# Optimization experiments

Hardware: AMD Instinct MI355X
Metric: run time of the kernel (lower is better)

## Reference

```python
import jax, jax.numpy as jnp
import numpy as np

B, N, F = 4, 3000, 128

def setup_inputs() -> dict:
    key = jax.random.key(0)
    k1, k2, k3, k4 = jax.random.split(key, 4)
    x = jax.random.normal(k1, (B, N, F), dtype=jnp.float32)
    adj = jax.random.uniform(k2, (B, N, N), dtype=jnp.float32)
    h0 = jax.random.normal(k3, (B, N, F), dtype=jnp.float32)
    stdv = 1.0 / np.sqrt(F)
    theta = jax.random.uniform(k4, (F, F), dtype=jnp.float32, minval=-stdv, maxval=stdv)
    return {
        "x": x, "adj": adj, "h0": h0, "theta": theta,
        "lamda": jnp.float32(0.5), "alpha": jnp.float32(0.1), "l": 4,
    }

def _normalize_adj(adj):
    # add self loops, then D^{-1/2} A D^{-1/2} via elementwise row/col scaling
    # (same math as diag-embed + inverse + two bmms in the original)
    n = adj.shape[1]
    adj = adj + jnp.eye(n, dtype=adj.dtype)
    deg = jnp.sum(adj, axis=2)                      # [B, N]
    d_inv_sqrt = jax.lax.rsqrt(deg)                 # [B, N]
    return d_inv_sqrt[:, :, None] * adj * d_inv_sqrt[:, None, :]

def reference(x, adj, h0, theta, lamda, alpha, l):
    adj_n = _normalize_adj(adj)
    beta = jnp.log(lamda / l + 1.0)
    hi = jnp.einsum('bnm,bmf->bnf', adj_n, x)       # aggregation
    support = (1.0 - alpha) * hi + alpha * h0       # variant=False path
    r = support
    out = beta * jnp.einsum('bnf,fg->bng', support, theta) + (1.0 - beta) * r
    return out
```

## Files before the change

### kernel.cpp

```cpp
#include <hip/hip_runtime.h>
#include <hip/hip_bf16.h>
#include <math.h>

#define BB 4
#define NN 3000
#define FF 128
#define NKC 94
#define NIT 188

typedef __bf16 bf16x8 __attribute__((ext_vector_type(8)));
typedef __bf16 bf16x4 __attribute__((ext_vector_type(4)));
typedef float  f32x4  __attribute__((ext_vector_type(4)));

__global__ __launch_bounds__(256) void k_deg(const float* __restrict__ adj,
                                             float* __restrict__ dis) {
    int wid  = (blockIdx.x * 256 + threadIdx.x) >> 6;
    int lane = threadIdx.x & 63;
    if (wid >= BB * NN) return;
    const float4* row = (const float4*)(adj + (size_t)wid * NN);
    float s = 0.f;
    for (int c = lane; c < NN / 4; c += 64) {
        float4 v = row[c];
        s += (v.x + v.y) + (v.z + v.w);
    }
    for (int off = 32; off > 0; off >>= 1) s += __shfl_down(s, off, 64);
    if (lane == 0) dis[wid] = 1.0f / sqrtf(s + 1.0f);
}

__global__ __launch_bounds__(256) void k_xpk(const float* __restrict__ x,
                                             const float* __restrict__ dis,
                                             __bf16* __restrict__ xpk) {
    int b  = blockIdx.y, kc = blockIdx.x;
    int t  = threadIdx.x, w = t >> 6, l = t & 63;
    int m  = l & 15, q = l >> 4;
    #pragma unroll
    for (int h = 0; h < 2; ++h) {
        int nt = w + h * 4;
        int f  = nt * 16 + m;
        bf16x8 v;
        #pragma unroll
        for (int j = 0; j < 8; ++j) {
            int k = kc * 32 + q * 8 + j;
            float val = 0.f;
            if (k < NN) val = dis[b * NN + k] * x[((size_t)b * NN + k) * FF + f];
            v[j] = (__bf16)val;
        }
        *(bf16x8*)(xpk + ((size_t)(b * 8 + nt) * NKC + kc) * 512 + l * 8) = v;
    }
}

__global__ __launch_bounds__(256) void k_thpk(const float* __restrict__ theta,
                                              __bf16* __restrict__ thpk) {
    int kc = blockIdx.x;
    int t  = threadIdx.x, w = t >> 6, l = t & 63;
    int m  = l & 15, q = l >> 4;
    #pragma unroll
    for (int h = 0; h < 2; ++h) {
        int nt = w + h * 4;
        bf16x8 v;
        #pragma unroll
        for (int j = 0; j < 8; ++j) {
            int k = kc * 32 + q * 8 + j;
            v[j] = (__bf16)theta[k * FF + nt * 16 + m];
        }
        *(bf16x8*)(thpk + ((size_t)(nt * 4 + kc)) * 512 + l * 8) = v;
    }
}

__global__ __launch_bounds__(256) void k_agg(const float* __restrict__ adj,
                                             const __bf16* __restrict__ xpk,
                                             const __bf16* __restrict__ thpk,
                                             const float* __restrict__ x,
                                             const float* __restrict__ h0,
                                             const float* __restrict__ dis,
                                             float* __restrict__ out,
                                             const float* __restrict__ alpha_p,
                                             const float* __restrict__ lamda_p,
                                             const int* __restrict__ l_p) {
    __shared__ __bf16 tile[16][264];
    const int b  = blockIdx.y;
    const int i0 = blockIdx.x * 16;
    const int t  = threadIdx.x, w = t >> 6, l = t & 63;
    const int m  = l & 15, quad = l >> 4;
    const int n0 = w * 32;
    const __bf16* B0 = xpk + ((size_t)(b * 8 + 2 * w) * NKC) * 512 + l * 8;
    const __bf16* B1 = B0 + (size_t)NKC * 512;
    f32x4 acc0 = {0.f, 0.f, 0.f, 0.f};
    f32x4 acc1 = {0.f, 0.f, 0.f, 0.f};
    for (int c = 0; c < 12; ++c) {
        int k0 = c * 256;
        #pragma unroll
        for (int i = 0; i < 4; ++i) {
            int row = i * 4 + w;
            int col = k0 + l * 4;
            float4 v = {0.f, 0.f, 0.f, 0.f};
            if (i0 + row < NN && col < NN)
                v = *(const float4*)(adj + ((size_t)b * NN + i0 + row) * NN + col);
            __bf16* tp = &tile[row][l * 4];
            tp[0] = (__bf16)v.x; tp[1] = (__bf16)v.y;
            tp[2] = (__bf16)v.z; tp[3] = (__bf16)v.w;
        }
        __syncthreads();
        int nk = (c == 11) ? 6 : 8;
        #pragma unroll 2
        for (int kcl = 0; kcl < nk; ++kcl) {
            int kc = c * 8 + kcl;
            bf16x8 a  = *(const bf16x8*)&tile[m][kcl * 32 + quad * 8];
            bf16x8 b0 = *(const bf16x8*)(B0 + (size_t)kc * 512);
            bf16x8 b1 = *(const bf16x8*)(B1 + (size_t)kc * 512);
            acc0 = __builtin_amdgcn_mfma_f32_16x16x32_bf16(a, b0, acc0, 0, 0, 0);
            acc1 = __builtin_amdgcn_mfma_f32_16x16x32_bf16(a, b1, acc1, 0, 0, 0);
        }
        __syncthreads();
    }
    const float alpha = *alpha_p;
    const float beta  = logf(*lamda_p / (float)(*l_p) + 1.0f);
    float s0v[4], s1v[4];
    #pragma unroll
    for (int r = 0; r < 4; ++r) {
        int row  = quad * 4 + r;
        int irow = i0 + row;
        float s0 = 0.f, s1 = 0.f;
        if (irow < NN) {
            float  di   = dis[b * NN + irow];
            size_t base = ((size_t)b * NN + irow) * FF;
            int c0 = n0 + m, c1 = n0 + 16 + m;
            s0 = (1.f - alpha) * (di * acc0[r] + di * di * x[base + c0]) + alpha * h0[base + c0];
            s1 = (1.f - alpha) * (di * acc1[r] + di * di * x[base + c1]) + alpha * h0[base + c1];
        }
        s0v[r] = s0; s1v[r] = s1;
        tile[row][n0 + m]      = (__bf16)s0;
        tile[row][n0 + 16 + m] = (__bf16)s1;
    }
    __syncthreads();
    f32x4 o0 = {0.f, 0.f, 0.f, 0.f};
    f32x4 o1 = {0.f, 0.f, 0.f, 0.f};
    const __bf16* T0 = thpk + (size_t)(2 * w * 4) * 512 + l * 8;
    const __bf16* T1 = T0 + 4 * 512;
    #pragma unroll
    for (int kc = 0; kc < 4; ++kc) {
        bf16x8 a   = *(const bf16x8*)&tile[m][kc * 32 + quad * 8];
        bf16x8 tb0 = *(const bf16x8*)(T0 + (size_t)kc * 512);
        bf16x8 tb1 = *(const bf16x8*)(T1 + (size_t)kc * 512);
        o0 = __builtin_amdgcn_mfma_f32_16x16x32_bf16(a, tb0, o0, 0, 0, 0);
        o1 = __builtin_amdgcn_mfma_f32_16x16x32_bf16(a, tb1, o1, 0, 0, 0);
    }
    const float omb = 1.f - beta;
    #pragma unroll
    for (int r = 0; r < 4; ++r) {
        int irow = i0 + quad * 4 + r;
        if (irow < NN) {
            size_t base = ((size_t)b * NN + irow) * FF;
            out[base + n0 + m]      = beta * o0[r] + omb * s0v[r];
            out[base + n0 + 16 + m] = beta * o1[r] + omb * s1v[r];
        }
    }
}

extern "C" void kernel_launch(void* const* d_in, const int* in_sizes, int n_in,
                              void* d_out, int out_size, void* d_ws, size_t ws_size,
                              hipStream_t stream) {
    const float* x      = (const float*)d_in[0];
    const float* adj    = (const float*)d_in[1];
    const float* h0     = (const float*)d_in[2];
    const float* theta  = (const float*)d_in[3];
    const float* lamda  = (const float*)d_in[4];
    const float* alpha  = (const float*)d_in[5];
    const int*   l      = (const int*)d_in[6];
    float* out = (float*)d_out;

    char*   ws   = (char*)d_ws;
    float*  dis  = (float*)ws;
    __bf16* xpk  = (__bf16*)(ws + 65536);
    __bf16* thpk = (__bf16*)(ws + 3200000);

    k_deg<<<dim3((BB * NN) / 4), 256, 0, stream>>>(adj, dis);
    k_xpk<<<dim3(NKC, BB), 256, 0, stream>>>(x, dis, xpk);
    k_thpk<<<dim3(4), 256, 0, stream>>>(theta, thpk);
    k_agg<<<dim3(NIT, BB), 256, 0, stream>>>(adj, xpk, thpk, x, h0, dis, out,
                                             alpha, lamda, l);
}
```

Measured before the change: 287.0 us.

## Fuse degree pass with bf16 MFMA-fragment packing of adjacency

The row-sum degree kernel is replaced by one that streams each 16-row adjacency tile once. It computes the row degrees and writes the tile as bf16 in the exact per-lane MFMA A-fragment layout. The aggregation kernel then loads A fragments straight from global memory, with no LDS staging, fp32-to-bf16 conversion or per-chunk barriers in its main loop. This moves the conversion work out of the GEMM loop and halves the bytes the GEMM reads for adjacency. In exchange it adds a 72 MB bf16 write and read-back through the workspace, which must be large enough to hold it.

```diff
diff --git a/kernel.cpp b/kernel.cpp
--- a/kernel.cpp
+++ b/kernel.cpp
@@ -9,22 +9,53 @@
 #define NIT 188
 
 typedef __bf16 bf16x8 __attribute__((ext_vector_type(8)));
-typedef __bf16 bf16x4 __attribute__((ext_vector_type(4)));
 typedef float  f32x4  __attribute__((ext_vector_type(4)));
 
-__global__ __launch_bounds__(256) void k_deg(const float* __restrict__ adj,
-                                             float* __restrict__ dis) {
-    int wid  = (blockIdx.x * 256 + threadIdx.x) >> 6;
-    int lane = threadIdx.x & 63;
-    if (wid >= BB * NN) return;
-    const float4* row = (const float4*)(adj + (size_t)wid * NN);
-    float s = 0.f;
-    for (int c = lane; c < NN / 4; c += 64) {
-        float4 v = row[c];
-        s += (v.x + v.y) + (v.z + v.w);
+__global__ __launch_bounds__(256) void k_degpack(const float* __restrict__ adj,
+                                                 __bf16* __restrict__ apk,
+                                                 float* __restrict__ dis) {
+    __shared__ float tile[16][260];
+    const int b  = blockIdx.y;
+    const int it = blockIdx.x;
+    const int i0 = it * 16;
+    const int t  = threadIdx.x, w = t >> 6, l = t & 63;
+    const int m  = l & 15, quad = l >> 4;
+    float dreg[4] = {0.f, 0.f, 0.f, 0.f};
+    __bf16* dst = apk + ((size_t)(b * NIT + it) * NKC) * 512 + l * 8;
+    for (int c = 0; c < 12; ++c) {
+        int k0 = c * 256;
+        #pragma unroll
+        for (int i = 0; i < 4; ++i) {
+            int row = i * 4 + w;
+            int col = k0 + l * 4;
+            float4 v = {0.f, 0.f, 0.f, 0.f};
+            if (i0 + row < NN && col < NN)
+                v = *(const float4*)(adj + ((size_t)b * NN + i0 + row) * NN + col);
+            dreg[i] += (v.x + v.y) + (v.z + v.w);
+            *(float4*)&tile[row][l * 4] = v;
+        }
+        __syncthreads();
+        int nk = (c == 11) ? 6 : 8;
+        #pragma unroll
+        for (int h = 0; h < 2; ++h) {
+            int kcl = w + h * 4;
+            if (kcl < nk) {
+                bf16x8 a;
+                #pragma unroll
+                for (int j = 0; j < 8; ++j)
+                    a[j] = (__bf16)tile[m][kcl * 32 + quad * 8 + j];
+                *(bf16x8*)(dst + (size_t)(c * 8 + kcl) * 512) = a;
+            }
+        }
+        __syncthreads();
     }
-    for (int off = 32; off > 0; off >>= 1) s += __shfl_down(s, off, 64);
-    if (lane == 0) dis[wid] = 1.0f / sqrtf(s + 1.0f);
+    #pragma unroll
+    for (int i = 0; i < 4; ++i) {
+        float s = dreg[i];
+        for (int off = 32; off > 0; off >>= 1) s += __shfl_down(s, off, 64);
+        int irow = i0 + i * 4 + w;
+        if (l == 0 && irow < NN) dis[b * NN + irow] = 1.0f / sqrtf(s + 1.0f);
+    }
 }
 
 __global__ __launch_bounds__(256) void k_xpk(const float* __restrict__ x,
@@ -67,7 +98,7 @@
     }
 }
 
-__global__ __launch_bounds__(256) void k_agg(const float* __restrict__ adj,
+__global__ __launch_bounds__(256) void k_agg(const __bf16* __restrict__ apk,
                                              const __bf16* __restrict__ xpk,
                                              const __bf16* __restrict__ thpk,
                                              const float* __restrict__ x,
@@ -77,41 +108,25 @@
                                              const float* __restrict__ alpha_p,
                                              const float* __restrict__ lamda_p,
                                              const int* __restrict__ l_p) {
-    __shared__ __bf16 tile[16][264];
+    __shared__ __bf16 stile[16][136];
     const int b  = blockIdx.y;
-    const int i0 = blockIdx.x * 16;
+    const int it = blockIdx.x;
+    const int i0 = it * 16;
     const int t  = threadIdx.x, w = t >> 6, l = t & 63;
     const int m  = l & 15, quad = l >> 4;
     const int n0 = w * 32;
+    const __bf16* Ap = apk + ((size_t)(b * NIT + it) * NKC) * 512 + l * 8;
     const __bf16* B0 = xpk + ((size_t)(b * 8 + 2 * w) * NKC) * 512 + l * 8;
     const __bf16* B1 = B0 + (size_t)NKC * 512;
     f32x4 acc0 = {0.f, 0.f, 0.f, 0.f};
     f32x4 acc1 = {0.f, 0.f, 0.f, 0.f};
-    for (int c = 0; c < 12; ++c) {
-        int k0 = c * 256;
-        #pragma unroll
-        for (int i = 0; i < 4; ++i) {
-            int row = i * 4 + w;
-            int col = k0 + l * 4;
-            float4 v = {0.f, 0.f, 0.f, 0.f};
-            if (i0 + row < NN && col < NN)
-                v = *(const float4*)(adj + ((size_t)b * NN + i0 + row) * NN + col);
-            __bf16* tp = &tile[row][l * 4];
-            tp[0] = (__bf16)v.x; tp[1] = (__bf16)v.y;
-            tp[2] = (__bf16)v.z; tp[3] = (__bf16)v.w;
-        }
-        __syncthreads();
-        int nk = (c == 11) ? 6 : 8;
-        #pragma unroll 2
-        for (int kcl = 0; kcl < nk; ++kcl) {
-            int kc = c * 8 + kcl;
-            bf16x8 a  = *(const bf16x8*)&tile[m][kcl * 32 + quad * 8];
-            bf16x8 b0 = *(const bf16x8*)(B0 + (size_t)kc * 512);
-            bf16x8 b1 = *(const bf16x8*)(B1 + (size_t)kc * 512);
-            acc0 = __builtin_amdgcn_mfma_f32_16x16x32_bf16(a, b0, acc0, 0, 0, 0);
-            acc1 = __builtin_amdgcn_mfma_f32_16x16x32_bf16(a, b1, acc1, 0, 0, 0);
-        }
-        __syncthreads();
+    #pragma unroll 2
+    for (int kc = 0; kc < NKC; ++kc) {
+        bf16x8 a  = *(const bf16x8*)(Ap + (size_t)kc * 512);
+        bf16x8 b0 = *(const bf16x8*)(B0 + (size_t)kc * 512);
+        bf16x8 b1 = *(const bf16x8*)(B1 + (size_t)kc * 512);
+        acc0 = __builtin_amdgcn_mfma_f32_16x16x32_bf16(a, b0, acc0, 0, 0, 0);
+        acc1 = __builtin_amdgcn_mfma_f32_16x16x32_bf16(a, b1, acc1, 0, 0, 0);
     }
     const float alpha = *alpha_p;
     const float beta  = logf(*lamda_p / (float)(*l_p) + 1.0f);
@@ -129,8 +144,8 @@
             s1 = (1.f - alpha) * (di * acc1[r] + di * di * x[base + c1]) + alpha * h0[base + c1];
         }
         s0v[r] = s0; s1v[r] = s1;
-        tile[row][n0 + m]      = (__bf16)s0;
-        tile[row][n0 + 16 + m] = (__bf16)s1;
+        stile[row][n0 + m]      = (__bf16)s0;
+        stile[row][n0 + 16 + m] = (__bf16)s1;
     }
     __syncthreads();
     f32x4 o0 = {0.f, 0.f, 0.f, 0.f};
@@ -139,7 +154,7 @@
     const __bf16* T1 = T0 + 4 * 512;
     #pragma unroll
     for (int kc = 0; kc < 4; ++kc) {
-        bf16x8 a   = *(const bf16x8*)&tile[m][kc * 32 + quad * 8];
+        bf16x8 a   = *(const bf16x8*)&stile[m][kc * 32 + quad * 8];
         bf16x8 tb0 = *(const bf16x8*)(T0 + (size_t)kc * 512);
         bf16x8 tb1 = *(const bf16x8*)(T1 + (size_t)kc * 512);
         o0 = __builtin_amdgcn_mfma_f32_16x16x32_bf16(a, tb0, o0, 0, 0, 0);
@@ -173,10 +188,11 @@
     float*  dis  = (float*)ws;
     __bf16* xpk  = (__bf16*)(ws + 65536);
     __bf16* thpk = (__bf16*)(ws + 3200000);
+    __bf16* apk  = (__bf16*)(ws + 4 * 1024 * 1024);
 
-    k_deg<<<dim3((BB * NN) / 4), 256, 0, stream>>>(adj, dis);
+    k_degpack<<<dim3(NIT, BB), 256, 0, stream>>>(adj, apk, dis);
+    k_thpk<<<dim3(4), 256, 0, stream>>>(theta, thpk);
     k_xpk<<<dim3(NKC, BB), 256, 0, stream>>>(x, dis, xpk);
-    k_thpk<<<dim3(4), 256, 0, stream>>>(theta, thpk);
-    k_agg<<<dim3(NIT, BB), 256, 0, stream>>>(adj, xpk, thpk, x, h0, dis, out,
+    k_agg<<<dim3(NIT, BB), 256, 0, stream>>>(apk, xpk, thpk, x, h0, dis, out,
                                              alpha, lamda, l);
 }
```

Result: no change. 287.3 us (+0.1%).

## Double-buffer adjacency tiles with register prefetch in aggregation kernel

Applied to the files above, without the earlier changes.

The aggregation kernel now uses two shared-memory buffers of 512 columns each. The next adjacency chunk is loaded into registers while MFMAs run on the current buffer, which halves the number of barriers and overlaps global loads with compute. NKC is padded to 96 so the chunk loop divides evenly, and zero-filled packed x covers the padding. Shared memory and register use go up, which may lower occupancy.

```diff
diff --git a/kernel.cpp b/kernel.cpp
--- a/kernel.cpp
+++ b/kernel.cpp
@@ -5,11 +5,10 @@
 #define BB 4
 #define NN 3000
 #define FF 128
-#define NKC 94
+#define NKC 96
 #define NIT 188
 
 typedef __bf16 bf16x8 __attribute__((ext_vector_type(8)));
-typedef __bf16 bf16x4 __attribute__((ext_vector_type(4)));
 typedef float  f32x4  __attribute__((ext_vector_type(4)));
 
 __global__ __launch_bounds__(256) void k_deg(const float* __restrict__ adj,
@@ -77,9 +76,11 @@
                                              const float* __restrict__ alpha_p,
                                              const float* __restrict__ lamda_p,
                                              const int* __restrict__ l_p) {
-    __shared__ __bf16 tile[16][264];
+    __shared__ __bf16 tile[2][16][520];
+    __shared__ __bf16 stile[16][136];
     const int b  = blockIdx.y;
-    const int i0 = blockIdx.x * 16;
+    const int it = blockIdx.x;
+    const int i0 = it * 16;
     const int t  = threadIdx.x, w = t >> 6, l = t & 63;
     const int m  = l & 15, quad = l >> 4;
     const int n0 = w * 32;
@@ -87,32 +88,56 @@
     const __bf16* B1 = B0 + (size_t)NKC * 512;
     f32x4 acc0 = {0.f, 0.f, 0.f, 0.f};
     f32x4 acc1 = {0.f, 0.f, 0.f, 0.f};
-    for (int c = 0; c < 12; ++c) {
-        int k0 = c * 256;
+
+    float4 pu[4], pv[4];
+    auto load_chunk = [&](int c) {
+        int k0 = c * 512;
+        #pragma unroll
+        for (int i = 0; i < 4; ++i) {
+            int row  = i * 4 + w;
+            int irow = i0 + row;
+            int col  = k0 + l * 8;
+            float4 u = {0.f, 0.f, 0.f, 0.f}, v = {0.f, 0.f, 0.f, 0.f};
+            if (irow < NN && col < NN) {
+                const float* p = adj + ((size_t)b * NN + irow) * NN + col;
+                u = *(const float4*)p;
+                v = *(const float4*)(p + 4);
+            }
+            pu[i] = u; pv[i] = v;
+        }
+    };
+    auto store_chunk = [&](int cb) {
         #pragma unroll
         for (int i = 0; i < 4; ++i) {
             int row = i * 4 + w;
-            int col = k0 + l * 4;
-            float4 v = {0.f, 0.f, 0.f, 0.f};
-            if (i0 + row < NN && col < NN)
-                v = *(const float4*)(adj + ((size_t)b * NN + i0 + row) * NN + col);
-            __bf16* tp = &tile[row][l * 4];
-            tp[0] = (__bf16)v.x; tp[1] = (__bf16)v.y;
-            tp[2] = (__bf16)v.z; tp[3] = (__bf16)v.w;
-        }
-        __syncthreads();
-        int nk = (c == 11) ? 6 : 8;
-        #pragma unroll 2
-        for (int kcl = 0; kcl < nk; ++kcl) {
-            int kc = c * 8 + kcl;
-            bf16x8 a  = *(const bf16x8*)&tile[m][kcl * 32 + quad * 8];
+            bf16x8 s;
+            s[0] = (__bf16)pu[i].x; s[1] = (__bf16)pu[i].y;
+            s[2] = (__bf16)pu[i].z; s[3] = (__bf16)pu[i].w;
+            s[4] = (__bf16)pv[i].x; s[5] = (__bf16)pv[i].y;
+            s[6] = (__bf16)pv[i].z; s[7] = (__bf16)pv[i].w;
+            *(bf16x8*)&tile[cb][row][l * 8] = s;
+        }
+    };
+
+    load_chunk(0);
+    store_chunk(0);
+    __syncthreads();
+    for (int c = 0; c < 6; ++c) {
+        int cb = c & 1;
+        if (c < 5) load_chunk(c + 1);
+        #pragma unroll 4
+        for (int kcl = 0; kcl < 16; ++kcl) {
+            int kc = c * 16 + kcl;
+            bf16x8 a  = *(const bf16x8*)&tile[cb][m][kcl * 32 + quad * 8];
             bf16x8 b0 = *(const bf16x8*)(B0 + (size_t)kc * 512);
             bf16x8 b1 = *(const bf16x8*)(B1 + (size_t)kc * 512);
             acc0 = __builtin_amdgcn_mfma_f32_16x16x32_bf16(a, b0, acc0, 0, 0, 0);
             acc1 = __builtin_amdgcn_mfma_f32_16x16x32_bf16(a, b1, acc1, 0, 0, 0);
         }
+        if (c < 5) store_chunk(cb ^ 1);
         __syncthreads();
     }
+
     const float alpha = *alpha_p;
     const float beta  = logf(*lamda_p / (float)(*l_p) + 1.0f);
     float s0v[4], s1v[4];
@@ -129,8 +154,8 @@
             s1 = (1.f - alpha) * (di * acc1[r] + di * di * x[base + c1]) + alpha * h0[base + c1];
         }
         s0v[r] = s0; s1v[r] = s1;
-        tile[row][n0 + m]      = (__bf16)s0;
-        tile[row][n0 + 16 + m] = (__bf16)s1;
+        stile[row][n0 + m]      = (__bf16)s0;
+        stile[row][n0 + 16 + m] = (__bf16)s1;
     }
     __syncthreads();
     f32x4 o0 = {0.f, 0.f, 0.f, 0.f};
@@ -139,7 +164,7 @@
     const __bf16* T1 = T0 + 4 * 512;
     #pragma unroll
     for (int kc = 0; kc < 4; ++kc) {
-        bf16x8 a   = *(const bf16x8*)&tile[m][kc * 32 + quad * 8];
+        bf16x8 a   = *(const bf16x8*)&stile[m][kc * 32 + quad * 8];
         bf16x8 tb0 = *(const bf16x8*)(T0 + (size_t)kc * 512);
         bf16x8 tb1 = *(const bf16x8*)(T1 + (size_t)kc * 512);
         o0 = __builtin_amdgcn_mfma_f32_16x16x32_bf16(a, tb0, o0, 0, 0, 0);
@@ -172,11 +197,11 @@
     char*   ws   = (char*)d_ws;
     float*  dis  = (float*)ws;
     __bf16* xpk  = (__bf16*)(ws + 65536);
-    __bf16* thpk = (__bf16*)(ws + 3200000);
+    __bf16* thpk = (__bf16*)(ws + 3276800);
 
     k_deg<<<dim3((BB * NN) / 4), 256, 0, stream>>>(adj, dis);
+    k_thpk<<<dim3(4), 256, 0, stream>>>(theta, thpk);
     k_xpk<<<dim3(NKC, BB), 256, 0, stream>>>(x, dis, xpk);
-    k_thpk<<<dim3(4), 256, 0, stream>>>(theta, thpk);
     k_agg<<<dim3(NIT, BB), 256, 0, stream>>>(adj, xpk, thpk, x, h0, dis, out,
                                              alpha, lamda, l);
 }
```

Result: faster. 277.1 us (-3.4%).
